# Optimization experiments

Hardware: AMD Instinct MI355X
Metric: run time of the kernel (lower is better)

The kernel has to match this reference:

```python
import jax, jax.numpy as jnp
import numpy as np

LN_EPS = 1e-5


def layer_norm(h, gamma, beta):
    m = jnp.mean(h, axis=-1, keepdims=True)
    v = jnp.mean((h - m) ** 2, axis=-1, keepdims=True)
    return (h - m) * jax.lax.rsqrt(v + LN_EPS) * gamma + beta


def setup_inputs() -> dict:
    key = jax.random.key(0)
    ks = jax.random.split(key, 4)
    B, N, D, H = 4, 256, 256, 256
    x = jax.random.normal(ks[0], (B, N, D), dtype=jnp.float32)
    # Linear(2D, H): weight stored as (in, out) for x @ W
    Wg = jax.random.normal(ks[1], (2 * D, H), dtype=jnp.float32) * (1.0 / np.sqrt(2 * D))
    bg = jnp.zeros((H,), dtype=jnp.float32)
    g_gamma = jnp.ones((H,), dtype=jnp.float32)
    g_beta = jnp.zeros((H,), dtype=jnp.float32)
    Wf = jax.random.normal(ks[2], (H, H), dtype=jnp.float32) * (1.0 / np.sqrt(H))
    bf = jnp.zeros((H,), dtype=jnp.float32)
    f_gamma = jnp.ones((H,), dtype=jnp.float32)
    f_beta = jnp.zeros((H,), dtype=jnp.float32)
    return {"x": x, "Wg": Wg, "bg": bg, "g_gamma": g_gamma, "g_beta": g_beta,
            "Wf": Wf, "bf": bf, "f_gamma": f_gamma, "f_beta": f_beta}


def reference(x, Wg, bg, g_gamma, g_beta, Wf, bf, f_gamma, f_beta):
    B, N, D = x.shape
    # Linear on concat([xi, xj]) == xi @ Wg[:D] + xj @ Wg[D:] ; avoids the (B,N,N,2D) cat.
    a = jnp.einsum('bnd,dh->bnh', x, Wg[:D])   # i-part
    b = jnp.einsum('bnd,dh->bnh', x, Wg[D:])   # j-part
    # pair pre-activation: (B, N_i, N_j, H)
    pre = a[:, :, None, :] + b[:, None, :, :] + bg
    r = layer_norm(jax.nn.relu(pre), g_gamma, g_beta)
    r = jnp.sum(r, axis=(1, 2))                # (B, H)
    rel = layer_norm(jax.nn.relu(r @ Wf + bf), f_gamma, f_beta)  # (B, H)
    return rel[:, None, :] + x                 # broadcast over N
```

## Files before the change

kernel.cpp:

```cpp
#include <hip/hip_runtime.h>

#define LN_EPS 1e-5f

constexpr int Bn = 4, Nn = 256, Dn = 256, Hn = 256;


__global__ __launch_bounds__(512) void gemm_ab_kernel(
    const float* __restrict__ x, const float* __restrict__ Wg,
    const float* __restrict__ bg, float* __restrict__ aA,
    float* __restrict__ bB, float* __restrict__ rC)
{
    int mt = blockIdx.x;
    int half = blockIdx.y;
    int m0 = mt * 4;
    int t = threadIdx.x;

    if (mt == 0 && half == 0) {
        for (int k = t; k < 1024; k += 512) rC[k] = 0.0f;
    }

    __shared__ float xs[4][256];
    __shared__ float accP[8][4][256];

    if (t < 256)
        reinterpret_cast<float4*>(&xs[0][0])[t] =
            reinterpret_cast<const float4*>(x + m0 * Dn)[t];
    __syncthreads();

    int h4 = t & 63;
    int dc = t >> 6;
    const float* Wp = Wg + (half ? Dn * Hn : 0) + h4 * 4;

    float4 acc[4];
#pragma unroll
    for (int m = 0; m < 4; ++m) acc[m] = make_float4(0.f, 0.f, 0.f, 0.f);

#pragma unroll 4
    for (int dd = 0; dd < 32; ++dd) {
        int d = dc * 32 + dd;
        float4 w = *reinterpret_cast<const float4*>(Wp + d * Hn);
#pragma unroll
        for (int m = 0; m < 4; ++m) {
            float xv = xs[m][d];
            acc[m].x = fmaf(xv, w.x, acc[m].x);
            acc[m].y = fmaf(xv, w.y, acc[m].y);
            acc[m].z = fmaf(xv, w.z, acc[m].z);
            acc[m].w = fmaf(xv, w.w, acc[m].w);
        }
    }
#pragma unroll
    for (int m = 0; m < 4; ++m)
        *reinterpret_cast<float4*>(&accP[dc][m][h4 * 4]) = acc[m];
    __syncthreads();

    int h = t & 255;
    int mh = t >> 8;
    float binit = half ? 0.0f : bg[h];
    float* outp = half ? bB : aA;
#pragma unroll
    for (int mi = 0; mi < 2; ++mi) {
        int m = mh * 2 + mi;
        float v = binit;
#pragma unroll
        for (int c = 0; c < 8; ++c) v += accP[c][m][h];
        outp[(m0 + m) * Hn + h] = v;
    }
}

__global__ __launch_bounds__(512, 2) void pair_kernel(
    const float* __restrict__ aA, const float* __restrict__ bB,
    float* __restrict__ rC, float* __restrict__ Cpart)
{
    const int b  = blockIdx.x >> 7;
    const int i0 = (blockIdx.x & 127) * 2;
    const int t  = threadIdx.x;

    __shared__ float Bs[32][260];
    __shared__ float invL[2][32];
    __shared__ float wred[8];

    const int jg = t >> 4;
    const int p  = t & 15;
    const int h4 = t & 63;
    const int c  = t >> 6;

    const float* aArow0 = aA + (b * Nn + i0) * Hn;
    const float* aArow1 = aArow0 + Hn;

    float4 As0[4], As1[4];
#pragma unroll
    for (int r = 0; r < 4; ++r) {
        As0[r] = *reinterpret_cast<const float4*>(aArow0 + 4 * (p + 16 * r));
        As1[r] = *reinterpret_cast<const float4*>(aArow1 + 4 * (p + 16 * r));
    }
    const float4 a0 = *reinterpret_cast<const float4*>(aArow0 + h4 * 4);
    const float4 a1 = *reinterpret_cast<const float4*>(aArow1 + h4 * 4);

    const float* browbase = bB + b * Nn * Hn;

    float4 acc0 = make_float4(0.f, 0.f, 0.f, 0.f);
    float4 acc1 = make_float4(0.f, 0.f, 0.f, 0.f);
    float Csum = 0.f;

    float4 bv[4], bvn[4];
    {
        const float* rp = browbase + jg * Hn;
#pragma unroll
        for (int r = 0; r < 4; ++r)
            bv[r] = *reinterpret_cast<const float4*>(rp + 4 * (p + 16 * r));
    }

    for (int jt = 0; jt < 8; ++jt) {
        float s0 = 0.f, q0 = 0.f, s1 = 0.f, q1 = 0.f;
#pragma unroll
        for (int r = 0; r < 4; ++r) {
            float v;
            v = fmaxf(As0[r].x + bv[r].x, 0.f); s0 += v; q0 = fmaf(v, v, q0);
            v = fmaxf(As0[r].y + bv[r].y, 0.f); s0 += v; q0 = fmaf(v, v, q0);
            v = fmaxf(As0[r].z + bv[r].z, 0.f); s0 += v; q0 = fmaf(v, v, q0);
            v = fmaxf(As0[r].w + bv[r].w, 0.f); s0 += v; q0 = fmaf(v, v, q0);
            v = fmaxf(As1[r].x + bv[r].x, 0.f); s1 += v; q1 = fmaf(v, v, q1);
            v = fmaxf(As1[r].y + bv[r].y, 0.f); s1 += v; q1 = fmaf(v, v, q1);
            v = fmaxf(As1[r].z + bv[r].z, 0.f); s1 += v; q1 = fmaf(v, v, q1);
            v = fmaxf(As1[r].w + bv[r].w, 0.f); s1 += v; q1 = fmaf(v, v, q1);
        }
#pragma unroll
        for (int r = 0; r < 4; ++r)
            *reinterpret_cast<float4*>(&Bs[jg][4 * (p + 16 * r)]) = bv[r];
        if (jt < 7) {
            const float* rp = browbase + ((jt + 1) * 32 + jg) * Hn;
#pragma unroll
            for (int r = 0; r < 4; ++r)
                bvn[r] = *reinterpret_cast<const float4*>(rp + 4 * (p + 16 * r));
        }
#pragma unroll
        for (int off = 8; off >= 1; off >>= 1) {
            s0 += __shfl_xor(s0, off, 16);
            q0 += __shfl_xor(q0, off, 16);
            s1 += __shfl_xor(s1, off, 16);
            q1 += __shfl_xor(q1, off, 16);
        }
        if (p == 0) {
            float m0 = s0 * (1.f / 256.f), m1 = s1 * (1.f / 256.f);
            float inv0 = rsqrtf(q0 * (1.f / 256.f) - m0 * m0 + LN_EPS);
            float inv1 = rsqrtf(q1 * (1.f / 256.f) - m1 * m1 + LN_EPS);
            invL[0][jg] = inv0;
            invL[1][jg] = inv1;
            Csum -= m0 * inv0 + m1 * inv1;
        }
        __syncthreads();
#pragma unroll
        for (int jj = 0; jj < 4; ++jj) {
            int j = c * 4 + jj;
            float w0 = invL[0][j];
            float w1 = invL[1][j];
            float4 b4 = *reinterpret_cast<const float4*>(&Bs[j][h4 * 4]);
            acc0.x = fmaf(w0, fmaxf(a0.x + b4.x, 0.f), acc0.x);
            acc0.y = fmaf(w0, fmaxf(a0.y + b4.y, 0.f), acc0.y);
            acc0.z = fmaf(w0, fmaxf(a0.z + b4.z, 0.f), acc0.z);
            acc0.w = fmaf(w0, fmaxf(a0.w + b4.w, 0.f), acc0.w);
            acc1.x = fmaf(w1, fmaxf(a1.x + b4.x, 0.f), acc1.x);
            acc1.y = fmaf(w1, fmaxf(a1.y + b4.y, 0.f), acc1.y);
            acc1.z = fmaf(w1, fmaxf(a1.z + b4.z, 0.f), acc1.z);
            acc1.w = fmaf(w1, fmaxf(a1.w + b4.w, 0.f), acc1.w);
        }
        __syncthreads();
#pragma unroll
        for (int r = 0; r < 4; ++r) bv[r] = bvn[r];
    }

    float* red = &Bs[0][0];
    *reinterpret_cast<float4*>(red + c * 256 + h4 * 4) = acc0;
    *reinterpret_cast<float4*>(red + (8 + c) * 256 + h4 * 4) = acc1;

    float cs = Csum;
#pragma unroll
    for (int off = 32; off >= 1; off >>= 1) cs += __shfl_xor(cs, off, 64);
    if ((t & 63) == 0) wred[t >> 6] = cs;
    __syncthreads();

    if (t < 256) {
        float v = 0.f;
#pragma unroll
        for (int cc = 0; cc < 8; ++cc)
            v += red[cc * 256 + t] + red[(8 + cc) * 256 + t];
        atomicAdd(&rC[b * Hn + t], v);
    }
    if (t == 0) {
        float cb = 0.f;
#pragma unroll
        for (int w = 0; w < 8; ++w) cb += wred[w];
        Cpart[blockIdx.x] = cb;
    }
}

__global__ __launch_bounds__(512) void finish_kernel(
    const float* __restrict__ rC, const float* __restrict__ Cpart,
    const float* __restrict__ gg, const float* __restrict__ gb,
    const float* __restrict__ Wf, const float* __restrict__ bfv,
    const float* __restrict__ fg, const float* __restrict__ fb,
    float* __restrict__ rel)
{
    const int b = blockIdx.x;
    const int t = threadIdx.x;
    __shared__ float rs[256];
    __shared__ float ysum[8][260];
    __shared__ float cred[2];
    __shared__ float pS[4], pQ[4];

    float cv = (t < 128) ? Cpart[b * 128 + t] : 0.f;
#pragma unroll
    for (int off = 32; off >= 1; off >>= 1) cv += __shfl_xor(cv, off, 64);
    if (t == 0 || t == 64) cred[t >> 6] = cv;
    __syncthreads();

    if (t < 256) {
        float Cb = cred[0] + cred[1];
        rs[t] = gg[t] * (rC[b * Hn + t] + Cb) + 65536.0f * gb[t];
    }
    __syncthreads();

    const int h4 = t & 63;
    const int kc = t >> 6;
    float4 acc = make_float4(0.f, 0.f, 0.f, 0.f);
    const float* Wp = Wf + h4 * 4;
#pragma unroll 8
    for (int kk = 0; kk < 32; ++kk) {
        int k = kc * 32 + kk;
        float4 w = *reinterpret_cast<const float4*>(Wp + k * Hn);
        float rv = rs[k];
        acc.x = fmaf(rv, w.x, acc.x);
        acc.y = fmaf(rv, w.y, acc.y);
        acc.z = fmaf(rv, w.z, acc.z);
        acc.w = fmaf(rv, w.w, acc.w);
    }
    *reinterpret_cast<float4*>(&ysum[kc][h4 * 4]) = acc;
    __syncthreads();

    float v = 0.f;
    if (t < 256) {
        v = bfv[t];
#pragma unroll
        for (int c = 0; c < 8; ++c) v += ysum[c][t];
        v = fmaxf(v, 0.f);
    }
    float sv = (t < 256) ? v : 0.f;
    float qv = (t < 256) ? v * v : 0.f;
#pragma unroll
    for (int off = 32; off >= 1; off >>= 1) {
        sv += __shfl_xor(sv, off, 64);
        qv += __shfl_xor(qv, off, 64);
    }
    if (t < 256 && (t & 63) == 0) { pS[t >> 6] = sv; pQ[t >> 6] = qv; }
    __syncthreads();

    if (t < 256) {
        float S = pS[0] + pS[1] + pS[2] + pS[3];
        float Q = pQ[0] + pQ[1] + pQ[2] + pQ[3];
        float m = S * (1.f / 256.f);
        float inv = rsqrtf(Q * (1.f / 256.f) - m * m + LN_EPS);
        rel[b * Hn + t] = (v - m) * inv * fg[t] + fb[t];
    }
}

__global__ __launch_bounds__(256) void add_kernel(
    const float* __restrict__ rel, const float* __restrict__ x,
    float* __restrict__ out)
{
    int idx = blockIdx.x * blockDim.x + threadIdx.x;
    int b = idx >> 14;
    int d4 = idx & 63;
    float4 r4 = reinterpret_cast<const float4*>(rel)[b * 64 + d4];
    float4 x4 = reinterpret_cast<const float4*>(x)[idx];
    float4 o;
    o.x = r4.x + x4.x;
    o.y = r4.y + x4.y;
    o.z = r4.z + x4.z;
    o.w = r4.w + x4.w;
    reinterpret_cast<float4*>(out)[idx] = o;
}

extern "C" void kernel_launch(void* const* d_in, const int* in_sizes, int n_in,
                              void* d_out, int out_size, void* d_ws, size_t ws_size,
                              hipStream_t stream)
{
    const float* x   = (const float*)d_in[0];
    const float* Wg  = (const float*)d_in[1];
    const float* bg  = (const float*)d_in[2];
    const float* gg  = (const float*)d_in[3];
    const float* gb  = (const float*)d_in[4];
    const float* Wf  = (const float*)d_in[5];
    const float* bfv = (const float*)d_in[6];
    const float* fg  = (const float*)d_in[7];
    const float* fb  = (const float*)d_in[8];
    float* out = (float*)d_out;

    float* ws    = (float*)d_ws;
    float* aA    = ws;
    float* bB    = ws + 262144;
    float* rC    = ws + 524288;
    float* Cpart = ws + 525312;
    float* rel   = ws + 525824;

    gemm_ab_kernel<<<dim3(256, 2), 512, 0, stream>>>(x, Wg, bg, aA, bB, rC);
    pair_kernel<<<512, 512, 0, stream>>>(aA, bB, rC, Cpart);
    finish_kernel<<<4, 512, 0, stream>>>(rC, Cpart, gg, gb, Wf, bfv, fg, fb, rel);
    add_kernel<<<256, 256, 0, stream>>>(rel, x, out);
}
```

Measured before the change: 103.2 us.

## Fuse pair, finish and add kernels via a grid-wide software barrier

Merges the pair-reduction, final linear+layernorm and residual-add kernels into one persistent kernel. All 512 blocks meet at an atomic-counter grid barrier, after which every block redundantly computes its batch's finish step and writes its own two output rows. This removes two kernel launches and the separate rel buffer. In exchange it relies on all 512 blocks being co-resident (launch bounds raised to 4 blocks per CU), repeats the Wf matvec in every block, and uses a spin barrier that can deadlock if residency is not met.

```diff
diff --git a/kernel.cpp b/kernel.cpp
--- a/kernel.cpp
+++ b/kernel.cpp
@@ -4,6 +4,9 @@
 
 constexpr int Bn = 4, Nn = 256, Dn = 256, Hn = 256;
 
+
+__device__ unsigned g_bar = 0;
+__device__ unsigned g_exit = 0;
 
 __global__ __launch_bounds__(512) void gemm_ab_kernel(
     const float* __restrict__ x, const float* __restrict__ Wg,
@@ -16,7 +19,7 @@
     int t = threadIdx.x;
 
     if (mt == 0 && half == 0) {
-        for (int k = t; k < 1024; k += 512) rC[k] = 0.0f;
+        for (int k = t; k < 1028; k += 512) rC[k] = 0.0f;
     }
 
     __shared__ float xs[4][256];
@@ -67,9 +70,13 @@
     }
 }
 
-__global__ __launch_bounds__(512, 2) void pair_kernel(
+__global__ __launch_bounds__(512, 4) void fused_pf_kernel(
     const float* __restrict__ aA, const float* __restrict__ bB,
-    float* __restrict__ rC, float* __restrict__ Cpart)
+    const float* __restrict__ x,
+    const float* __restrict__ gg, const float* __restrict__ gb,
+    const float* __restrict__ Wf, const float* __restrict__ bfv,
+    const float* __restrict__ fg, const float* __restrict__ fb,
+    float* __restrict__ rC, float* __restrict__ out)
 {
     const int b  = blockIdx.x >> 7;
     const int i0 = (blockIdx.x & 127) * 2;
@@ -78,180 +85,184 @@
     __shared__ float Bs[32][260];
     __shared__ float invL[2][32];
     __shared__ float wred[8];
+    __shared__ float rs[256];
+    __shared__ float relS[256];
+    __shared__ float ysum[8][260];
+    __shared__ float pS[4], pQ[4];
+    __shared__ float cbuf;
 
     const int jg = t >> 4;
     const int p  = t & 15;
     const int h4 = t & 63;
     const int c  = t >> 6;
 
-    const float* aArow0 = aA + (b * Nn + i0) * Hn;
-    const float* aArow1 = aArow0 + Hn;
-
-    float4 As0[4], As1[4];
-#pragma unroll
-    for (int r = 0; r < 4; ++r) {
-        As0[r] = *reinterpret_cast<const float4*>(aArow0 + 4 * (p + 16 * r));
-        As1[r] = *reinterpret_cast<const float4*>(aArow1 + 4 * (p + 16 * r));
-    }
-    const float4 a0 = *reinterpret_cast<const float4*>(aArow0 + h4 * 4);
-    const float4 a1 = *reinterpret_cast<const float4*>(aArow1 + h4 * 4);
-
-    const float* browbase = bB + b * Nn * Hn;
-
-    float4 acc0 = make_float4(0.f, 0.f, 0.f, 0.f);
-    float4 acc1 = make_float4(0.f, 0.f, 0.f, 0.f);
-    float Csum = 0.f;
-
-    float4 bv[4], bvn[4];
     {
-        const float* rp = browbase + jg * Hn;
-#pragma unroll
-        for (int r = 0; r < 4; ++r)
-            bv[r] = *reinterpret_cast<const float4*>(rp + 4 * (p + 16 * r));
-    }
-
-    for (int jt = 0; jt < 8; ++jt) {
-        float s0 = 0.f, q0 = 0.f, s1 = 0.f, q1 = 0.f;
+        const float* aArow0 = aA + (b * Nn + i0) * Hn;
+        const float* aArow1 = aArow0 + Hn;
+
+        float4 As0[4], As1[4];
 #pragma unroll
         for (int r = 0; r < 4; ++r) {
-            float v;
-            v = fmaxf(As0[r].x + bv[r].x, 0.f); s0 += v; q0 = fmaf(v, v, q0);
-            v = fmaxf(As0[r].y + bv[r].y, 0.f); s0 += v; q0 = fmaf(v, v, q0);
-            v = fmaxf(As0[r].z + bv[r].z, 0.f); s0 += v; q0 = fmaf(v, v, q0);
-            v = fmaxf(As0[r].w + bv[r].w, 0.f); s0 += v; q0 = fmaf(v, v, q0);
-            v = fmaxf(As1[r].x + bv[r].x, 0.f); s1 += v; q1 = fmaf(v, v, q1);
-            v = fmaxf(As1[r].y + bv[r].y, 0.f); s1 += v; q1 = fmaf(v, v, q1);
-            v = fmaxf(As1[r].z + bv[r].z, 0.f); s1 += v; q1 = fmaf(v, v, q1);
-            v = fmaxf(As1[r].w + bv[r].w, 0.f); s1 += v; q1 = fmaf(v, v, q1);
-        }
-#pragma unroll
-        for (int r = 0; r < 4; ++r)
-            *reinterpret_cast<float4*>(&Bs[jg][4 * (p + 16 * r)]) = bv[r];
-        if (jt < 7) {
-            const float* rp = browbase + ((jt + 1) * 32 + jg) * Hn;
+            As0[r] = *reinterpret_cast<const float4*>(aArow0 + 4 * (p + 16 * r));
+            As1[r] = *reinterpret_cast<const float4*>(aArow1 + 4 * (p + 16 * r));
+        }
+        const float4 a0 = *reinterpret_cast<const float4*>(aArow0 + h4 * 4);
+        const float4 a1 = *reinterpret_cast<const float4*>(aArow1 + h4 * 4);
+
+        const float* browbase = bB + b * Nn * Hn;
+
+        float4 acc0 = make_float4(0.f, 0.f, 0.f, 0.f);
+        float4 acc1 = make_float4(0.f, 0.f, 0.f, 0.f);
+        float Csum = 0.f;
+
+        float4 bv[4], bvn[4];
+        {
+            const float* rp = browbase + jg * Hn;
 #pragma unroll
             for (int r = 0; r < 4; ++r)
-                bvn[r] = *reinterpret_cast<const float4*>(rp + 4 * (p + 16 * r));
-        }
-#pragma unroll
-        for (int off = 8; off >= 1; off >>= 1) {
-            s0 += __shfl_xor(s0, off, 16);
-            q0 += __shfl_xor(q0, off, 16);
-            s1 += __shfl_xor(s1, off, 16);
-            q1 += __shfl_xor(q1, off, 16);
-        }
-        if (p == 0) {
-            float m0 = s0 * (1.f / 256.f), m1 = s1 * (1.f / 256.f);
-            float inv0 = rsqrtf(q0 * (1.f / 256.f) - m0 * m0 + LN_EPS);
-            float inv1 = rsqrtf(q1 * (1.f / 256.f) - m1 * m1 + LN_EPS);
-            invL[0][jg] = inv0;
-            invL[1][jg] = inv1;
-            Csum -= m0 * inv0 + m1 * inv1;
-        }
+                bv[r] = *reinterpret_cast<const float4*>(rp + 4 * (p + 16 * r));
+        }
+
+        for (int jt = 0; jt < 8; ++jt) {
+            float s0 = 0.f, q0 = 0.f, s1 = 0.f, q1 = 0.f;
+#pragma unroll
+            for (int r = 0; r < 4; ++r) {
+                float v;
+                v = fmaxf(As0[r].x + bv[r].x, 0.f); s0 += v; q0 = fmaf(v, v, q0);
+                v = fmaxf(As0[r].y + bv[r].y, 0.f); s0 += v; q0 = fmaf(v, v, q0);
+                v = fmaxf(As0[r].z + bv[r].z, 0.f); s0 += v; q0 = fmaf(v, v, q0);
+                v = fmaxf(As0[r].w + bv[r].w, 0.f); s0 += v; q0 = fmaf(v, v, q0);
+                v = fmaxf(As1[r].x + bv[r].x, 0.f); s1 += v; q1 = fmaf(v, v, q1);
+                v = fmaxf(As1[r].y + bv[r].y, 0.f); s1 += v; q1 = fmaf(v, v, q1);
+                v = fmaxf(As1[r].z + bv[r].z, 0.f); s1 += v; q1 = fmaf(v, v, q1);
+                v = fmaxf(As1[r].w + bv[r].w, 0.f); s1 += v; q1 = fmaf(v, v, q1);
+            }
+#pragma unroll
+            for (int r = 0; r < 4; ++r)
+                *reinterpret_cast<float4*>(&Bs[jg][4 * (p + 16 * r)]) = bv[r];
+            if (jt < 7) {
+                const float* rp = browbase + ((jt + 1) * 32 + jg) * Hn;
+#pragma unroll
+                for (int r = 0; r < 4; ++r)
+                    bvn[r] = *reinterpret_cast<const float4*>(rp + 4 * (p + 16 * r));
+            }
+#pragma unroll
+            for (int off = 8; off >= 1; off >>= 1) {
+                s0 += __shfl_xor(s0, off, 16);
+                q0 += __shfl_xor(q0, off, 16);
+                s1 += __shfl_xor(s1, off, 16);
+                q1 += __shfl_xor(q1, off, 16);
+            }
+            if (p == 0) {
+                float m0 = s0 * (1.f / 256.f), m1 = s1 * (1.f / 256.f);
+                float inv0 = rsqrtf(q0 * (1.f / 256.f) - m0 * m0 + LN_EPS);
+                float inv1 = rsqrtf(q1 * (1.f / 256.f) - m1 * m1 + LN_EPS);
+                invL[0][jg] = inv0;
+                invL[1][jg] = inv1;
+                Csum -= m0 * inv0 + m1 * inv1;
+            }
+            __syncthreads();
+#pragma unroll
+            for (int jj = 0; jj < 4; ++jj) {
+                int j = c * 4 + jj;
+                float w0 = invL[0][j];
+                float w1 = invL[1][j];
+                float4 b4 = *reinterpret_cast<const float4*>(&Bs[j][h4 * 4]);
+                acc0.x = fmaf(w0, fmaxf(a0.x + b4.x, 0.f), acc0.x);
+                acc0.y = fmaf(w0, fmaxf(a0.y + b4.y, 0.f), acc0.y);
+                acc0.z = fmaf(w0, fmaxf(a0.z + b4.z, 0.f), acc0.z);
+                acc0.w = fmaf(w0, fmaxf(a0.w + b4.w, 0.f), acc0.w);
+                acc1.x = fmaf(w1, fmaxf(a1.x + b4.x, 0.f), acc1.x);
+                acc1.y = fmaf(w1, fmaxf(a1.y + b4.y, 0.f), acc1.y);
+                acc1.z = fmaf(w1, fmaxf(a1.z + b4.z, 0.f), acc1.z);
+                acc1.w = fmaf(w1, fmaxf(a1.w + b4.w, 0.f), acc1.w);
+            }
+            __syncthreads();
+#pragma unroll
+            for (int r = 0; r < 4; ++r) bv[r] = bvn[r];
+        }
+
+        float* red = &Bs[0][0];
+        *reinterpret_cast<float4*>(red + c * 256 + h4 * 4) = acc0;
+        *reinterpret_cast<float4*>(red + (8 + c) * 256 + h4 * 4) = acc1;
+
+        float cs = Csum;
+#pragma unroll
+        for (int off = 32; off >= 1; off >>= 1) cs += __shfl_xor(cs, off, 64);
+        if ((t & 63) == 0) wred[t >> 6] = cs;
         __syncthreads();
-#pragma unroll
-        for (int jj = 0; jj < 4; ++jj) {
-            int j = c * 4 + jj;
-            float w0 = invL[0][j];
-            float w1 = invL[1][j];
-            float4 b4 = *reinterpret_cast<const float4*>(&Bs[j][h4 * 4]);
-            acc0.x = fmaf(w0, fmaxf(a0.x + b4.x, 0.f), acc0.x);
-            acc0.y = fmaf(w0, fmaxf(a0.y + b4.y, 0.f), acc0.y);
-            acc0.z = fmaf(w0, fmaxf(a0.z + b4.z, 0.f), acc0.z);
-            acc0.w = fmaf(w0, fmaxf(a0.w + b4.w, 0.f), acc0.w);
-            acc1.x = fmaf(w1, fmaxf(a1.x + b4.x, 0.f), acc1.x);
-            acc1.y = fmaf(w1, fmaxf(a1.y + b4.y, 0.f), acc1.y);
-            acc1.z = fmaf(w1, fmaxf(a1.z + b4.z, 0.f), acc1.z);
-            acc1.w = fmaf(w1, fmaxf(a1.w + b4.w, 0.f), acc1.w);
-        }
-        __syncthreads();
-#pragma unroll
-        for (int r = 0; r < 4; ++r) bv[r] = bvn[r];
-    }
-
-    float* red = &Bs[0][0];
-    *reinterpret_cast<float4*>(red + c * 256 + h4 * 4) = acc0;
-    *reinterpret_cast<float4*>(red + (8 + c) * 256 + h4 * 4) = acc1;
-
-    float cs = Csum;
-#pragma unroll
-    for (int off = 32; off >= 1; off >>= 1) cs += __shfl_xor(cs, off, 64);
-    if ((t & 63) == 0) wred[t >> 6] = cs;
-    __syncthreads();
-
-    if (t < 256) {
-        float v = 0.f;
-#pragma unroll
-        for (int cc = 0; cc < 8; ++cc)
-            v += red[cc * 256 + t] + red[(8 + cc) * 256 + t];
-        atomicAdd(&rC[b * Hn + t], v);
-    }
+
+        if (t < 256) {
+            float v = 0.f;
+#pragma unroll
+            for (int cc = 0; cc < 8; ++cc)
+                v += red[cc * 256 + t] + red[(8 + cc) * 256 + t];
+            atomicAdd(&rC[b * Hn + t], v);
+        }
+        if (t == 0) {
+            float cb = 0.f;
+#pragma unroll
+            for (int w = 0; w < 8; ++w) cb += wred[w];
+            atomicAdd(&rC[1024 + b], cb);
+        }
+    }
+
+    __syncthreads();
     if (t == 0) {
-        float cb = 0.f;
-#pragma unroll
-        for (int w = 0; w < 8; ++w) cb += wred[w];
-        Cpart[blockIdx.x] = cb;
-    }
-}
-
-__global__ __launch_bounds__(512) void finish_kernel(
-    const float* __restrict__ rC, const float* __restrict__ Cpart,
-    const float* __restrict__ gg, const float* __restrict__ gb,
-    const float* __restrict__ Wf, const float* __restrict__ bfv,
-    const float* __restrict__ fg, const float* __restrict__ fb,
-    float* __restrict__ rel)
-{
-    const int b = blockIdx.x;
-    const int t = threadIdx.x;
-    __shared__ float rs[256];
-    __shared__ float ysum[8][260];
-    __shared__ float cred[2];
-    __shared__ float pS[4], pQ[4];
-
-    float cv = (t < 128) ? Cpart[b * 128 + t] : 0.f;
-#pragma unroll
-    for (int off = 32; off >= 1; off >>= 1) cv += __shfl_xor(cv, off, 64);
-    if (t == 0 || t == 64) cred[t >> 6] = cv;
-    __syncthreads();
-
-    if (t < 256) {
-        float Cb = cred[0] + cred[1];
-        rs[t] = gg[t] * (rC[b * Hn + t] + Cb) + 65536.0f * gb[t];
-    }
-    __syncthreads();
-
-    const int h4 = t & 63;
-    const int kc = t >> 6;
-    float4 acc = make_float4(0.f, 0.f, 0.f, 0.f);
-    const float* Wp = Wf + h4 * 4;
+        __threadfence();
+        atomicAdd(&g_bar, 1u);
+        while (atomicAdd(&g_bar, 0u) < 512u) __builtin_amdgcn_s_sleep(8);
+        __threadfence();
+        unsigned e = atomicAdd(&g_exit, 1u);
+        if (e == 511u) {
+            atomicExch(&g_bar, 0u);
+            atomicExch(&g_exit, 0u);
+        }
+    }
+    __syncthreads();
+
+    float rraw = 0.f;
+    if (t == 0) cbuf = atomicAdd(&rC[1024 + b], 0.0f);
+    if (t < 256) rraw = atomicAdd(&rC[b * Hn + t], 0.0f);
+    __syncthreads();
+    if (t < 256) rs[t] = gg[t] * (rraw + cbuf) + 65536.0f * gb[t];
+    __syncthreads();
+
+    {
+        const int kc = t >> 6;
+        float4 acc = make_float4(0.f, 0.f, 0.f, 0.f);
+        const float* Wp = Wf + h4 * 4;
 #pragma unroll 8
-    for (int kk = 0; kk < 32; ++kk) {
-        int k = kc * 32 + kk;
-        float4 w = *reinterpret_cast<const float4*>(Wp + k * Hn);
-        float rv = rs[k];
-        acc.x = fmaf(rv, w.x, acc.x);
-        acc.y = fmaf(rv, w.y, acc.y);
-        acc.z = fmaf(rv, w.z, acc.z);
-        acc.w = fmaf(rv, w.w, acc.w);
-    }
-    *reinterpret_cast<float4*>(&ysum[kc][h4 * 4]) = acc;
+        for (int kk = 0; kk < 32; ++kk) {
+            int k = kc * 32 + kk;
+            float4 w = *reinterpret_cast<const float4*>(Wp + k * Hn);
+            float rv = rs[k];
+            acc.x = fmaf(rv, w.x, acc.x);
+            acc.y = fmaf(rv, w.y, acc.y);
+            acc.z = fmaf(rv, w.z, acc.z);
+            acc.w = fmaf(rv, w.w, acc.w);
+        }
+        *reinterpret_cast<float4*>(&ysum[kc][h4 * 4]) = acc;
+    }
     __syncthreads();
 
     float v = 0.f;
     if (t < 256) {
         v = bfv[t];
 #pragma unroll
-        for (int c = 0; c < 8; ++c) v += ysum[c][t];
+        for (int cc = 0; cc < 8; ++cc) v += ysum[cc][t];
         v = fmaxf(v, 0.f);
     }
-    float sv = (t < 256) ? v : 0.f;
-    float qv = (t < 256) ? v * v : 0.f;
-#pragma unroll
-    for (int off = 32; off >= 1; off >>= 1) {
-        sv += __shfl_xor(sv, off, 64);
-        qv += __shfl_xor(qv, off, 64);
-    }
-    if (t < 256 && (t & 63) == 0) { pS[t >> 6] = sv; pQ[t >> 6] = qv; }
+    {
+        float sv = (t < 256) ? v : 0.f;
+        float qv = (t < 256) ? v * v : 0.f;
+#pragma unroll
+        for (int off = 32; off >= 1; off >>= 1) {
+            sv += __shfl_xor(sv, off, 64);
+            qv += __shfl_xor(qv, off, 64);
+        }
+        if (t < 256 && (t & 63) == 0) { pS[t >> 6] = sv; pQ[t >> 6] = qv; }
+    }
     __syncthreads();
 
     if (t < 256) {
@@ -259,25 +270,24 @@
         float Q = pQ[0] + pQ[1] + pQ[2] + pQ[3];
         float m = S * (1.f / 256.f);
         float inv = rsqrtf(Q * (1.f / 256.f) - m * m + LN_EPS);
-        rel[b * Hn + t] = (v - m) * inv * fg[t] + fb[t];
-    }
-}
-
-__global__ __launch_bounds__(256) void add_kernel(
-    const float* __restrict__ rel, const float* __restrict__ x,
-    float* __restrict__ out)
-{
-    int idx = blockIdx.x * blockDim.x + threadIdx.x;
-    int b = idx >> 14;
-    int d4 = idx & 63;
-    float4 r4 = reinterpret_cast<const float4*>(rel)[b * 64 + d4];
-    float4 x4 = reinterpret_cast<const float4*>(x)[idx];
-    float4 o;
-    o.x = r4.x + x4.x;
-    o.y = r4.y + x4.y;
-    o.z = r4.z + x4.z;
-    o.w = r4.w + x4.w;
-    reinterpret_cast<float4*>(out)[idx] = o;
+        relS[t] = (v - m) * inv * fg[t] + fb[t];
+    }
+    __syncthreads();
+
+    if (t < 128) {
+        int nsl = blockIdx.x & 127;
+        int row = nsl * 2 + (t >> 6);
+        int col4 = t & 63;
+        int idx = (b * Nn + row) * (Hn / 4) + col4;
+        float4 xv = reinterpret_cast<const float4*>(x)[idx];
+        float4 r4 = *reinterpret_cast<const float4*>(&relS[col4 * 4]);
+        float4 o;
+        o.x = xv.x + r4.x;
+        o.y = xv.y + r4.y;
+        o.z = xv.z + r4.z;
+        o.w = xv.w + r4.w;
+        reinterpret_cast<float4*>(out)[idx] = o;
+    }
 }
 
 extern "C" void kernel_launch(void* const* d_in, const int* in_sizes, int n_in,
@@ -295,15 +305,12 @@
     const float* fb  = (const float*)d_in[8];
     float* out = (float*)d_out;
 
-    float* ws    = (float*)d_ws;
-    float* aA    = ws;
-    float* bB    = ws + 262144;
-    float* rC    = ws + 524288;
-    float* Cpart = ws + 525312;
-    float* rel   = ws + 525824;
+    float* ws = (float*)d_ws;
+    float* aA = ws;
+    float* bB = ws + 262144;
+    float* rC = ws + 524288;
 
     gemm_ab_kernel<<<dim3(256, 2), 512, 0, stream>>>(x, Wg, bg, aA, bB, rC);
-    pair_kernel<<<512, 512, 0, stream>>>(aA, bB, rC, Cpart);
-    finish_kernel<<<4, 512, 0, stream>>>(rC, Cpart, gg, gb, Wf, bfv, fg, fb, rel);
-    add_kernel<<<256, 256, 0, stream>>>(rel, x, out);
+    fused_pf_kernel<<<512, 512, 0, stream>>>(aA, bB, x, gg, gb, Wf, bfv,
+                                             fg, fb, rC, out);
 }
```

After: 144.4 us. 40.0% more time.

## Keep relu values in registers and reduce pair accumulators with wave shuffles

Applied to the files above, without the earlier changes.

Restructures the pair kernel so each thread owns a fixed 16-wide slice of H for both i rows, keeps the relu values in registers, and applies the per-row LN scale directly. This removes the shared-memory staging of B rows, the two barriers per j-tile and the recomputation of relu(a+b). Partial sums across j are reduced with cross-lane shuffles and a small padded shared buffer before the atomics. In exchange it uses more registers, drops the software prefetch of the next B tile, and adds a redundant zero-valued atomicAdd per thread, doubling the number of atomics.

```diff
diff --git a/kernel.cpp b/kernel.cpp
--- a/kernel.cpp
+++ b/kernel.cpp
@@ -74,122 +74,142 @@
     const int b  = blockIdx.x >> 7;
     const int i0 = (blockIdx.x & 127) * 2;
     const int t  = threadIdx.x;
-
-    __shared__ float Bs[32][260];
-    __shared__ float invL[2][32];
+    const int s  = t >> 4;
+    const int p  = t & 15;
+
+    __shared__ float fred[8][16][33];
     __shared__ float wred[8];
 
-    const int jg = t >> 4;
-    const int p  = t & 15;
-    const int h4 = t & 63;
-    const int c  = t >> 6;
-
-    const float* aArow0 = aA + (b * Nn + i0) * Hn;
+    const float* aArow0 = aA + (b * Nn + i0) * Hn + p * 16;
     const float* aArow1 = aArow0 + Hn;
-
-    float4 As0[4], As1[4];
+    float4 A0[4], A1[4];
 #pragma unroll
     for (int r = 0; r < 4; ++r) {
-        As0[r] = *reinterpret_cast<const float4*>(aArow0 + 4 * (p + 16 * r));
-        As1[r] = *reinterpret_cast<const float4*>(aArow1 + 4 * (p + 16 * r));
-    }
-    const float4 a0 = *reinterpret_cast<const float4*>(aArow0 + h4 * 4);
-    const float4 a1 = *reinterpret_cast<const float4*>(aArow1 + h4 * 4);
-
-    const float* browbase = bB + b * Nn * Hn;
-
-    float4 acc0 = make_float4(0.f, 0.f, 0.f, 0.f);
-    float4 acc1 = make_float4(0.f, 0.f, 0.f, 0.f);
+        A0[r] = *reinterpret_cast<const float4*>(aArow0 + r * 4);
+        A1[r] = *reinterpret_cast<const float4*>(aArow1 + r * 4);
+    }
+
+    const float* bbase = bB + b * Nn * Hn + p * 16;
+
+    float4 acc0[4], acc1[4];
+#pragma unroll
+    for (int r = 0; r < 4; ++r) {
+        acc0[r] = make_float4(0.f, 0.f, 0.f, 0.f);
+        acc1[r] = make_float4(0.f, 0.f, 0.f, 0.f);
+    }
     float Csum = 0.f;
 
-    float4 bv[4], bvn[4];
-    {
-        const float* rp = browbase + jg * Hn;
+    for (int jt = 0; jt < 8; ++jt) {
+        const int j = jt * 32 + s;
+        const float* rp = bbase + j * Hn;
+        float4 bv[4];
 #pragma unroll
         for (int r = 0; r < 4; ++r)
-            bv[r] = *reinterpret_cast<const float4*>(rp + 4 * (p + 16 * r));
-    }
-
-    for (int jt = 0; jt < 8; ++jt) {
+            bv[r] = *reinterpret_cast<const float4*>(rp + r * 4);
+
+        float4 v0[4], v1[4];
         float s0 = 0.f, q0 = 0.f, s1 = 0.f, q1 = 0.f;
 #pragma unroll
         for (int r = 0; r < 4; ++r) {
-            float v;
-            v = fmaxf(As0[r].x + bv[r].x, 0.f); s0 += v; q0 = fmaf(v, v, q0);
-            v = fmaxf(As0[r].y + bv[r].y, 0.f); s0 += v; q0 = fmaf(v, v, q0);
-            v = fmaxf(As0[r].z + bv[r].z, 0.f); s0 += v; q0 = fmaf(v, v, q0);
-            v = fmaxf(As0[r].w + bv[r].w, 0.f); s0 += v; q0 = fmaf(v, v, q0);
-            v = fmaxf(As1[r].x + bv[r].x, 0.f); s1 += v; q1 = fmaf(v, v, q1);
-            v = fmaxf(As1[r].y + bv[r].y, 0.f); s1 += v; q1 = fmaf(v, v, q1);
-            v = fmaxf(As1[r].z + bv[r].z, 0.f); s1 += v; q1 = fmaf(v, v, q1);
-            v = fmaxf(As1[r].w + bv[r].w, 0.f); s1 += v; q1 = fmaf(v, v, q1);
-        }
-#pragma unroll
-        for (int r = 0; r < 4; ++r)
-            *reinterpret_cast<float4*>(&Bs[jg][4 * (p + 16 * r)]) = bv[r];
-        if (jt < 7) {
-            const float* rp = browbase + ((jt + 1) * 32 + jg) * Hn;
-#pragma unroll
-            for (int r = 0; r < 4; ++r)
-                bvn[r] = *reinterpret_cast<const float4*>(rp + 4 * (p + 16 * r));
-        }
-#pragma unroll
-        for (int off = 8; off >= 1; off >>= 1) {
+            float4 w;
+            w.x = fmaxf(A0[r].x + bv[r].x, 0.f);
+            w.y = fmaxf(A0[r].y + bv[r].y, 0.f);
+            w.z = fmaxf(A0[r].z + bv[r].z, 0.f);
+            w.w = fmaxf(A0[r].w + bv[r].w, 0.f);
+            v0[r] = w;
+            s0 += w.x + w.y + w.z + w.w;
+            q0 = fmaf(w.x, w.x, q0); q0 = fmaf(w.y, w.y, q0);
+            q0 = fmaf(w.z, w.z, q0); q0 = fmaf(w.w, w.w, q0);
+            float4 u;
+            u.x = fmaxf(A1[r].x + bv[r].x, 0.f);
+            u.y = fmaxf(A1[r].y + bv[r].y, 0.f);
+            u.z = fmaxf(A1[r].z + bv[r].z, 0.f);
+            u.w = fmaxf(A1[r].w + bv[r].w, 0.f);
+            v1[r] = u;
+            s1 += u.x + u.y + u.z + u.w;
+            q1 = fmaf(u.x, u.x, q1); q1 = fmaf(u.y, u.y, q1);
+            q1 = fmaf(u.z, u.z, q1); q1 = fmaf(u.w, u.w, q1);
+        }
+#pragma unroll
+        for (int off = 1; off <= 8; off <<= 1) {
             s0 += __shfl_xor(s0, off, 16);
             q0 += __shfl_xor(q0, off, 16);
             s1 += __shfl_xor(s1, off, 16);
             q1 += __shfl_xor(q1, off, 16);
         }
-        if (p == 0) {
-            float m0 = s0 * (1.f / 256.f), m1 = s1 * (1.f / 256.f);
-            float inv0 = rsqrtf(q0 * (1.f / 256.f) - m0 * m0 + LN_EPS);
-            float inv1 = rsqrtf(q1 * (1.f / 256.f) - m1 * m1 + LN_EPS);
-            invL[0][jg] = inv0;
-            invL[1][jg] = inv1;
-            Csum -= m0 * inv0 + m1 * inv1;
-        }
-        __syncthreads();
-#pragma unroll
-        for (int jj = 0; jj < 4; ++jj) {
-            int j = c * 4 + jj;
-            float w0 = invL[0][j];
-            float w1 = invL[1][j];
-            float4 b4 = *reinterpret_cast<const float4*>(&Bs[j][h4 * 4]);
-            acc0.x = fmaf(w0, fmaxf(a0.x + b4.x, 0.f), acc0.x);
-            acc0.y = fmaf(w0, fmaxf(a0.y + b4.y, 0.f), acc0.y);
-            acc0.z = fmaf(w0, fmaxf(a0.z + b4.z, 0.f), acc0.z);
-            acc0.w = fmaf(w0, fmaxf(a0.w + b4.w, 0.f), acc0.w);
-            acc1.x = fmaf(w1, fmaxf(a1.x + b4.x, 0.f), acc1.x);
-            acc1.y = fmaf(w1, fmaxf(a1.y + b4.y, 0.f), acc1.y);
-            acc1.z = fmaf(w1, fmaxf(a1.z + b4.z, 0.f), acc1.z);
-            acc1.w = fmaf(w1, fmaxf(a1.w + b4.w, 0.f), acc1.w);
-        }
-        __syncthreads();
-#pragma unroll
-        for (int r = 0; r < 4; ++r) bv[r] = bvn[r];
-    }
-
-    float* red = &Bs[0][0];
-    *reinterpret_cast<float4*>(red + c * 256 + h4 * 4) = acc0;
-    *reinterpret_cast<float4*>(red + (8 + c) * 256 + h4 * 4) = acc1;
-
+        float m0 = s0 * (1.f / 256.f), m1 = s1 * (1.f / 256.f);
+        float inv0 = rsqrtf(q0 * (1.f / 256.f) - m0 * m0 + LN_EPS);
+        float inv1 = rsqrtf(q1 * (1.f / 256.f) - m1 * m1 + LN_EPS);
+        if (p == 0) Csum -= m0 * inv0 + m1 * inv1;
+#pragma unroll
+        for (int r = 0; r < 4; ++r) {
+            acc0[r].x = fmaf(inv0, v0[r].x, acc0[r].x);
+            acc0[r].y = fmaf(inv0, v0[r].y, acc0[r].y);
+            acc0[r].z = fmaf(inv0, v0[r].z, acc0[r].z);
+            acc0[r].w = fmaf(inv0, v0[r].w, acc0[r].w);
+            acc1[r].x = fmaf(inv1, v1[r].x, acc1[r].x);
+            acc1[r].y = fmaf(inv1, v1[r].y, acc1[r].y);
+            acc1[r].z = fmaf(inv1, v1[r].z, acc1[r].z);
+            acc1[r].w = fmaf(inv1, v1[r].w, acc1[r].w);
+        }
+    }
+
+#pragma unroll
+    for (int r = 0; r < 4; ++r) {
+        acc0[r].x += __shfl_xor(acc0[r].x, 16, 64);
+        acc0[r].y += __shfl_xor(acc0[r].y, 16, 64);
+        acc0[r].z += __shfl_xor(acc0[r].z, 16, 64);
+        acc0[r].w += __shfl_xor(acc0[r].w, 16, 64);
+        acc1[r].x += __shfl_xor(acc1[r].x, 16, 64);
+        acc1[r].y += __shfl_xor(acc1[r].y, 16, 64);
+        acc1[r].z += __shfl_xor(acc1[r].z, 16, 64);
+        acc1[r].w += __shfl_xor(acc1[r].w, 16, 64);
+    }
+#pragma unroll
+    for (int r = 0; r < 4; ++r) {
+        acc0[r].x += __shfl_xor(acc0[r].x, 32, 64);
+        acc0[r].y += __shfl_xor(acc0[r].y, 32, 64);
+        acc0[r].z += __shfl_xor(acc0[r].z, 32, 64);
+        acc0[r].w += __shfl_xor(acc0[r].w, 32, 64);
+        acc1[r].x += __shfl_xor(acc1[r].x, 32, 64);
+        acc1[r].y += __shfl_xor(acc1[r].y, 32, 64);
+        acc1[r].z += __shfl_xor(acc1[r].z, 32, 64);
+        acc1[r].w += __shfl_xor(acc1[r].w, 32, 64);
+    }
+    const int w = t >> 6;
+    if ((t & 63) < 16) {
+#pragma unroll
+        for (int r = 0; r < 4; ++r) {
+            fred[w][p][r * 4 + 0] = acc0[r].x;
+            fred[w][p][r * 4 + 1] = acc0[r].y;
+            fred[w][p][r * 4 + 2] = acc0[r].z;
+            fred[w][p][r * 4 + 3] = acc0[r].w;
+            fred[w][p][16 + r * 4 + 0] = acc1[r].x;
+            fred[w][p][16 + r * 4 + 1] = acc1[r].y;
+            fred[w][p][16 + r * 4 + 2] = acc1[r].z;
+            fred[w][p][16 + r * 4 + 3] = acc1[r].w;
+        }
+    }
     float cs = Csum;
 #pragma unroll
     for (int off = 32; off >= 1; off >>= 1) cs += __shfl_xor(cs, off, 64);
-    if ((t & 63) == 0) wred[t >> 6] = cs;
-    __syncthreads();
-
-    if (t < 256) {
+    if ((t & 63) == 0) wred[w] = cs;
+    __syncthreads();
+
+    {
+        const int i  = t >> 8;
+        const int h  = t & 255;
+        const int pp = h >> 4, hh = h & 15;
         float v = 0.f;
 #pragma unroll
-        for (int cc = 0; cc < 8; ++cc)
-            v += red[cc * 256 + t] + red[(8 + cc) * 256 + t];
-        atomicAdd(&rC[b * Hn + t], v);
+        for (int ww = 0; ww < 8; ++ww) v += fred[ww][pp][i * 16 + hh];
+        atomicAdd(&rC[(b * Nn + 0) * 0 + b * Hn + h + i * 0], 0.0f);
+        atomicAdd(&rC[b * Hn + h], v);
     }
     if (t == 0) {
         float cb = 0.f;
 #pragma unroll
-        for (int w = 0; w < 8; ++w) cb += wred[w];
+        for (int ww = 0; ww < 8; ++ww) cb += wred[ww];
         Cpart[blockIdx.x] = cb;
     }
 }
```

New measurement: 117.0 us. +13.4%, slower.
